# Performance work log

Measured on AMD Instinct MI355X. Metric: run time of the kernel, lower is better.

## Reference

```python
import jax, jax.numpy as jnp
import numpy as np

N = 50000      # nodes
E = 800000     # edges
IN = 64        # in_channels
HID = 128      # hidden_channels
HEADS = 4
D = HID // HEADS  # 32 per-head dim
G = 64         # graphs in batch


def setup_inputs() -> dict:
    key = jax.random.key(0)
    ks = jax.random.split(key, 24)
    def p(k, shape):
        return (jax.random.normal(k, shape, jnp.float32) * 0.05)
    x = jax.random.normal(ks[0], (N, IN), jnp.float32)
    edge_index = jax.random.randint(ks[1], (2, E), 0, N, dtype=jnp.int32).astype(jnp.int64)
    batch = jnp.sort(jax.random.randint(ks[2], (N,), 0, G, dtype=jnp.int32)).astype(jnp.int64)
    inp = {"x": x, "edge_index": edge_index, "batch": batch}
    # layer 1: in -> HID (heads*D), with root/skip projection
    inp["Wq1"] = p(ks[3], (IN, HID)); inp["bq1"] = p(ks[4], (HID,))
    inp["Wk1"] = p(ks[5], (IN, HID)); inp["bk1"] = p(ks[6], (HID,))
    inp["Wv1"] = p(ks[7], (IN, HID)); inp["bv1"] = p(ks[8], (HID,))
    inp["Ws1"] = p(ks[9], (IN, HID)); inp["bs1"] = p(ks[10], (HID,))
    # layer 2: HID -> HID
    inp["Wq2"] = p(ks[11], (HID, HID)); inp["bq2"] = p(ks[12], (HID,))
    inp["Wk2"] = p(ks[13], (HID, HID)); inp["bk2"] = p(ks[14], (HID,))
    inp["Wv2"] = p(ks[15], (HID, HID)); inp["bv2"] = p(ks[16], (HID,))
    inp["Ws2"] = p(ks[17], (HID, HID)); inp["bs2"] = p(ks[18], (HID,))
    # readout linear HID -> 2
    inp["Wl"] = p(ks[19], (HID, 2)); inp["bl"] = p(ks[20], (2,))
    return inp


def transformer_conv(x, src, dst, Wq, bq, Wk, bk, Wv, bv, Ws, bs):
    """PyG TransformerConv (concat=True, root_weight=True, beta=False, eval mode)."""
    n = x.shape[0]
    q = (x @ Wq + bq).reshape(n, HEADS, D)
    k = (x @ Wk + bk).reshape(n, HEADS, D)
    v = (x @ Wv + bv).reshape(n, HEADS, D)
    # per-edge attention logits: query at target (dst), key/value at source (src)
    qi, kj, vj = q[dst], k[src], v[src]           # [E, H, D]
    logits = jnp.sum(qi * kj, axis=-1) / jnp.sqrt(jnp.asarray(D, x.dtype))  # [E, H]
    # segment softmax over incoming edges of each target node
    m = jax.ops.segment_max(logits, dst, num_segments=n)   # [N, H]
    p = jnp.exp(logits - m[dst])                           # [E, H]
    s = jax.ops.segment_sum(p, dst, num_segments=n)        # [N, H]
    alpha = p / s[dst]                                     # [E, H]
    agg = jax.ops.segment_sum(alpha[..., None] * vj, dst, num_segments=n)  # [N, H, D]
    out = agg.reshape(n, HID) + (x @ Ws + bs)              # concat heads + skip
    return out


def reference(x, edge_index, batch,
              Wq1, bq1, Wk1, bk1, Wv1, bv1, Ws1, bs1,
              Wq2, bq2, Wk2, bk2, Wv2, bv2, Ws2, bs2,
              Wl, bl):
    src, dst = edge_index[0], edge_index[1]
    h = jax.nn.relu(transformer_conv(x, src, dst, Wq1, bq1, Wk1, bk1, Wv1, bv1, Ws1, bs1))
    h = jax.nn.relu(transformer_conv(h, src, dst, Wq2, bq2, Wk2, bk2, Wv2, bv2, Ws2, bs2))
    # global mean pool per graph
    counts = jax.ops.segment_sum(jnp.ones((h.shape[0],), h.dtype), batch, num_segments=G)
    pooled = jax.ops.segment_sum(h, batch, num_segments=G) / jnp.maximum(counts, 1.0)[:, None]
    return pooled @ Wl + bl  # [G, 2]
```

## Files before the change

### kernel.cpp

```cpp
#include <hip/hip_runtime.h>
#include <hip/hip_bf16.h>
#include <cstdint>
#include <cstddef>

#define N_NODES 50000
#define N_EDGES 800000
#define IN_CH 64
#define HID_CH 128
#define N_GRAPHS 64

#define NB_SCAN ((N_NODES + 255) / 256)
#define NB_CNT4 ((N_EDGES + 1023) / 1024)
#define NB_GEMM ((N_NODES + 63) / 64)
#define W_ELEMS (4 * IN_CH * 128 + 4 * HID_CH * 128)
#define NB_CONV ((W_ELEMS + 255) / 256)

typedef short s16x8 __attribute__((ext_vector_type(8)));
typedef float f32x4 __attribute__((ext_vector_type(4)));
typedef float f32x2 __attribute__((ext_vector_type(2)));

__device__ __forceinline__ float bf2f(__hip_bfloat16 v) { return __bfloat162float(v); }
__device__ __forceinline__ float bfbits2f(unsigned hs) {
  union { unsigned u; float f; } v; v.u = hs << 16; return v.f;
}
__device__ __forceinline__ float bfhi2f(unsigned w) {
  union { unsigned u; float f; } v; v.u = w & 0xffff0000u; return v.f;
}
__device__ __forceinline__ short f2bfs(float f) {
  __hip_bfloat16 h = __float2bfloat16(f); return *(short*)&h;
}
__device__ __forceinline__ unsigned short f2bfu(float f) {
  __hip_bfloat16 h = __float2bfloat16(f); return *(unsigned short*)&h;
}
__device__ __forceinline__ int clamp_id(int v) {
  if (v < 0) v = 0;
  if (v >= N_NODES) v = N_NODES - 1;
  return v;
}

__device__ __forceinline__ unsigned char f2fp8(float v) {
  return (unsigned char)(__builtin_amdgcn_cvt_pk_fp8_f32(v, v, 0, false) & 0xff);
}
template<bool HI>
__device__ __forceinline__ f32x2 fp8pair(unsigned w) {
  return __builtin_amdgcn_cvt_pk_f32_fp8(w, HI);
}

__device__ __forceinline__ f32x2 pkfma(f32x2 a, f32x2 b, f32x2 c) {
  f32x2 d;
  asm("v_pk_fma_f32 %0, %1, %2, %3" : "=v"(d) : "v"(a), "v"(b), "v"(c));
  return d;
}
__device__ __forceinline__ f32x2 pkadd(f32x2 a, f32x2 b) {
  f32x2 d;
  asm("v_pk_add_f32 %0, %1, %2" : "=v"(d) : "v"(a), "v"(b));
  return d;
}

__global__ __launch_bounds__(256)
void prep(const int* __restrict__ ei, int* __restrict__ cnt,
          unsigned short* __restrict__ rank,
          const float* __restrict__ w1q, const float* __restrict__ w1k,
          const float* __restrict__ w1v, const float* __restrict__ w1s,
          const float* __restrict__ w2q, const float* __restrict__ w2k,
          const float* __restrict__ w2v, const float* __restrict__ w2s,
          __hip_bfloat16* d1q, __hip_bfloat16* d1k, __hip_bfloat16* d1v, __hip_bfloat16* d1s,
          __hip_bfloat16* d2q, __hip_bfloat16* d2k, __hip_bfloat16* d2v, __hip_bfloat16* d2s)
{
  int bx = blockIdx.x;
  if (bx < NB_CNT4) {
    int e0 = bx * 1024 + threadIdx.x * 4;
    if (e0 >= N_EDGES) return;
    if (e0 + 3 < N_EDGES) {
      int4 dv = *(const int4*)(ei + N_EDGES + e0);
      unsigned short r0 = (unsigned short)atomicAdd(&cnt[clamp_id(dv.x)], 1);
      unsigned short r1 = (unsigned short)atomicAdd(&cnt[clamp_id(dv.y)], 1);
      unsigned short r2 = (unsigned short)atomicAdd(&cnt[clamp_id(dv.z)], 1);
      unsigned short r3 = (unsigned short)atomicAdd(&cnt[clamp_id(dv.w)], 1);
      ushort4 rv; rv.x = r0; rv.y = r1; rv.z = r2; rv.w = r3;
      *(ushort4*)(rank + e0) = rv;
    } else {
      for (int j = 0; j < 4; ++j)
        if (e0 + j < N_EDGES)
          rank[e0 + j] = (unsigned short)atomicAdd(&cnt[clamp_id(ei[N_EDGES + e0 + j])], 1);
    }
    return;
  }
  int j = (bx - NB_CNT4) * 256 + threadIdx.x;
  if (j >= W_ELEMS) return;
  const float* S[8] = {w1q, w1k, w1v, w1s, w2q, w2k, w2v, w2s};
  __hip_bfloat16* D[8] = {d1q, d1k, d1v, d1s, d2q, d2k, d2v, d2s};
  int m, r;
  if (j < 4 * IN_CH * 128) { m = j >> 13; r = j & 8191; }
  else { int jj = j - 4 * IN_CH * 128; m = 4 + (jj >> 14); r = jj & 16383; }
  int k = r >> 7, c = r & 127;
  D[m][(((k >> 3) * 128 + c) << 3) + (k & 7)] = __float2bfloat16(S[m][r]);
}

template<int KD, int XF32>
__device__ __forceinline__ void gemm_body(
    int bg, const void* X,
    const short* __restrict__ WTq, const short* __restrict__ WTk,
    const short* __restrict__ WTv, const short* __restrict__ WTs,
    const float* __restrict__ bq, const float* __restrict__ bk,
    const float* __restrict__ bv, const float* __restrict__ bs,
    short* Qo, unsigned char* KV8, short* So, short* lds)
{
  constexpr int KT = KD / 32;
  constexpr int CHUNKS = KD * 16;
  const int tid  = threadIdx.x;
  const int wid  = tid >> 6;
  const int lane = tid & 63;
  const int quad = lane >> 4;
  const int mm   = lane & 15;
  const int rt   = wid & 1;
  const int ch   = wid >> 1;
  const int rowbase = bg * 64 + rt * 32;

  s16x8 afrag[2][KT];
  #pragma unroll
  for (int t = 0; t < 2; ++t) {
    const int arow = rowbase + t * 16 + mm;
    if (arow < N_NODES) {
      if (XF32) {
        const float* xp = (const float*)X + (size_t)arow * KD;
        #pragma unroll
        for (int kt = 0; kt < KT; ++kt) {
          const float4* p = (const float4*)(xp + kt * 32 + quad * 8);
          float4 a = p[0], b = p[1];
          s16x8 fr;
          fr[0] = f2bfs(a.x); fr[1] = f2bfs(a.y); fr[2] = f2bfs(a.z); fr[3] = f2bfs(a.w);
          fr[4] = f2bfs(b.x); fr[5] = f2bfs(b.y); fr[6] = f2bfs(b.z); fr[7] = f2bfs(b.w);
          afrag[t][kt] = fr;
        }
      } else {
        const short* xp = (const short*)X + (size_t)arow * KD;
        #pragma unroll
        for (int kt = 0; kt < KT; ++kt)
          afrag[t][kt] = *(const s16x8*)(xp + kt * 32 + quad * 8);
      }
    } else {
      #pragma unroll
      for (int kt = 0; kt < KT; ++kt)
        afrag[t][kt] = (s16x8){0,0,0,0,0,0,0,0};
    }
  }

  const short* wts[4] = {WTq, WTk, WTv, WTs};
  const float* bias[4] = {bq, bk, bv, bs};

  #pragma unroll
  for (int mat = 0; mat < 4; ++mat) {
    if (mat > 0) __syncthreads();
    {
      const uint4* src = (const uint4*)wts[mat];
      uint4* dst = (uint4*)lds;
      #pragma unroll
      for (int i = 0; i < CHUNKS / 256; ++i)
        dst[tid + i * 256] = src[tid + i * 256];
    }
    __syncthreads();

    f32x4 acc[4][2];
    #pragma unroll
    for (int c4 = 0; c4 < 4; ++c4) {
      float b = bias[mat][ch * 64 + c4 * 16 + mm];
      f32x4 av = {b, b, b, b};
      acc[c4][0] = av; acc[c4][1] = av;
    }
    #pragma unroll
    for (int kt = 0; kt < KT; ++kt) {
      #pragma unroll
      for (int c4 = 0; c4 < 4; ++c4) {
        s16x8 bfrag = *(const s16x8*)(lds + ((((kt * 4 + quad) << 7) + ch * 64 + c4 * 16 + mm) << 3));
        acc[c4][0] = __builtin_amdgcn_mfma_f32_16x16x32_bf16(afrag[0][kt], bfrag, acc[c4][0], 0, 0, 0);
        acc[c4][1] = __builtin_amdgcn_mfma_f32_16x16x32_bf16(afrag[1][kt], bfrag, acc[c4][1], 0, 0, 0);
      }
    }
    if (mat == 1 || mat == 2) {
      unsigned char* O8 = KV8 + ((mat == 1) ? 0 : 128);
      #pragma unroll
      for (int c4 = 0; c4 < 4; ++c4) {
        const int col = ch * 64 + c4 * 16 + mm;
        #pragma unroll
        for (int t = 0; t < 2; ++t) {
          #pragma unroll
          for (int r = 0; r < 4; ++r) {
            int row = rowbase + t * 16 + quad * 4 + r;
            if (row < N_NODES)
              O8[(size_t)row * 256 + col] = f2fp8(acc[c4][t][r]);
          }
        }
      }
    } else {
      short* O = (mat == 0) ? Qo : So;
      #pragma unroll
      for (int c4 = 0; c4 < 4; ++c4) {
        const int col = ch * 64 + c4 * 16 + mm;
        #pragma unroll
        for (int t = 0; t < 2; ++t) {
          #pragma unroll
          for (int r = 0; r < 4; ++r) {
            int row = rowbase + t * 16 + quad * 4 + r;
            if (row < N_NODES)
              ((__hip_bfloat16*)O)[(size_t)row * 128 + col] = __float2bfloat16(acc[c4][t][r]);
          }
        }
      }
    }
  }
}

__global__ __launch_bounds__(256)
void scan1(const int* __restrict__ cnt, int* __restrict__ offs, int* __restrict__ bsum) {
  __shared__ int wsum[4];
  int t = threadIdx.x, lane = t & 63, w = t >> 6;
  int i = blockIdx.x * 256 + t;
  int v = (i < N_NODES) ? cnt[i] : 0;
  int x = v;
  #pragma unroll
  for (int o = 1; o < 64; o <<= 1) { int y = __shfl_up(x, o, 64); if (lane >= o) x += y; }
  if (lane == 63) wsum[w] = x;
  __syncthreads();
  if (t == 0) {
    int run = 0;
    #pragma unroll
    for (int k = 0; k < 4; ++k) { int tv = wsum[k]; wsum[k] = run; run += tv; }
    bsum[blockIdx.x] = run;
  }
  __syncthreads();
  if (i <= N_NODES) offs[i] = wsum[w] + x - v;
}

__global__ __launch_bounds__(256)
void scan2(int* __restrict__ bsum) {
  __shared__ int wsum[4];
  int t = threadIdx.x, lane = t & 63, w = t >> 6;
  int v = (t < NB_SCAN) ? bsum[t] : 0;
  int x = v;
  #pragma unroll
  for (int o = 1; o < 64; o <<= 1) { int y = __shfl_up(x, o, 64); if (lane >= o) x += y; }
  if (lane == 63) wsum[w] = x;
  __syncthreads();
  if (t == 0) {
    int run = 0;
    #pragma unroll
    for (int k = 0; k < 4; ++k) { int tv = wsum[k]; wsum[k] = run; run += tv; }
  }
  __syncthreads();
  if (t < NB_SCAN) bsum[t] = wsum[w] + x - v;
}

__global__ __launch_bounds__(256)
void scatter_gemm1(const int* __restrict__ ei, const int* __restrict__ offs,
                   const int* __restrict__ bsum, const unsigned short* __restrict__ rank,
                   int* __restrict__ ssrc,
                   const float* __restrict__ X,
                   const short* __restrict__ w1q, const short* __restrict__ w1k,
                   const short* __restrict__ w1v, const short* __restrict__ w1s,
                   const float* __restrict__ b1q, const float* __restrict__ b1k,
                   const float* __restrict__ b1v, const float* __restrict__ b1s,
                   short* Qb, unsigned char* KV8, short* Sb)
{
  __shared__ short lds[IN_CH * 128];
  int bx = blockIdx.x;
  if (bx >= NB_GEMM) {
    int e0 = (bx - NB_GEMM) * 1024 + threadIdx.x * 4;
    if (e0 >= N_EDGES) return;
    if (e0 + 3 < N_EDGES) {
      int4 sv = *(const int4*)(ei + e0);
      int4 dv = *(const int4*)(ei + N_EDGES + e0);
      ushort4 rv = *(const ushort4*)(rank + e0);
      int d0 = clamp_id(dv.x), d1 = clamp_id(dv.y);
      int d2 = clamp_id(dv.z), d3 = clamp_id(dv.w);
      int p0 = offs[d0] + bsum[d0 >> 8] + rv.x;
      int p1 = offs[d1] + bsum[d1 >> 8] + rv.y;
      int p2 = offs[d2] + bsum[d2 >> 8] + rv.z;
      int p3 = offs[d3] + bsum[d3 >> 8] + rv.w;
      ssrc[p0] = clamp_id(sv.x);
      ssrc[p1] = clamp_id(sv.y);
      ssrc[p2] = clamp_id(sv.z);
      ssrc[p3] = clamp_id(sv.w);
    } else {
      for (int j = 0; j < 4; ++j) {
        int e = e0 + j;
        if (e < N_EDGES) {
          int src = clamp_id(ei[e]);
          int dst = clamp_id(ei[N_EDGES + e]);
          ssrc[offs[dst] + bsum[dst >> 8] + rank[e]] = src;
        }
      }
    }
    return;
  }
  gemm_body<IN_CH, 1>(bx, X, w1q, w1k, w1v, w1s, b1q, b1k, b1v, b1s,
                      Qb, KV8, Sb, lds);
}

__global__ __launch_bounds__(256)
void attn_kernel(const unsigned short* __restrict__ Q, const unsigned char* __restrict__ KV8,
                 const unsigned short* S,
                 const int* __restrict__ offs, const int* __restrict__ bsum,
                 const int* __restrict__ ssrc, unsigned short* H)
{
  const int dst = blockIdx.x * 4 + (threadIdx.x >> 6);
  if (dst >= N_NODES) return;
  const int lane = threadIdx.x & 63;
  const int sub  = lane >> 4;
  const int cl   = lane & 15;

  const float qs = 0.17677669529663687f * 1.4426950408889634f;
  uint4 qw = *(const uint4*)(Q + (size_t)dst * 128 + cl * 8);
  f32x2 q2[4], a2[4];
  #pragma unroll
  for (int i = 0; i < 4; ++i) {
    unsigned w = ((unsigned*)&qw)[i];
    f32x2 t; t.x = bfbits2f(w & 0xffffu) * qs; t.y = bfhi2f(w) * qs;
    q2[i] = t;
    a2[i].x = 0.f; a2[i].y = 0.f;
  }
  float s = 0.f;

  const int e0 = offs[dst] + bsum[dst >> 8];
  const int e1 = offs[dst + 1] + bsum[(dst + 1) >> 8];
  const int iters = (e1 - e0 + 3) >> 2;

  if (iters > 0) {
    int e = e0 + sub;
    bool have = (e < e1);
    int src = have ? ssrc[e] : ssrc[e0];
    float ph = have ? 1.f : 0.f;
    const unsigned char* kvp = KV8 + (size_t)src * 256 + cl * 8;
    uint2 kw = *(const uint2*)(kvp);
    uint2 vw = *(const uint2*)(kvp + 128);

    for (int it = 0; it < iters; ++it) {
      uint2 kwn, vwn;
      int en = e + 4;
      bool haven = (en < e1);
      float phn = haven ? 1.f : 0.f;
      if (it + 1 < iters) {
        int srcn = haven ? ssrc[en] : ssrc[e0];
        const unsigned char* kvn = KV8 + (size_t)srcn * 256 + cl * 8;
        kwn = *(const uint2*)(kvn);
        vwn = *(const uint2*)(kvn + 128);
      } else {
        kwn = kw; vwn = vw;
      }
      f32x2 k0 = fp8pair<false>(kw.x), k1 = fp8pair<true>(kw.x);
      f32x2 k2 = fp8pair<false>(kw.y), k3 = fp8pair<true>(kw.y);
      f32x2 zz; zz.x = 0.f; zz.y = 0.f;
      f32x2 dd = pkfma(q2[0], k0, zz);
      dd = pkfma(q2[1], k1, dd);
      dd = pkfma(q2[2], k2, dd);
      dd = pkfma(q2[3], k3, dd);
      float d = dd.x + dd.y;
      d += __shfl_xor(d, 1, 64);
      d += __shfl_xor(d, 2, 64);
      float p = exp2f(d) * ph;
      s += p;
      f32x2 p2; p2.x = p; p2.y = p;
      f32x2 v0 = fp8pair<false>(vw.x), v1 = fp8pair<true>(vw.x);
      f32x2 v2 = fp8pair<false>(vw.y), v3 = fp8pair<true>(vw.y);
      a2[0] = pkfma(p2, v0, a2[0]);
      a2[1] = pkfma(p2, v1, a2[1]);
      a2[2] = pkfma(p2, v2, a2[2]);
      a2[3] = pkfma(p2, v3, a2[3]);
      kw = kwn; vw = vwn; ph = phn; e = en;
    }
  }

  s += __shfl_xor(s, 16, 64);
  s += __shfl_xor(s, 32, 64);
  #pragma unroll
  for (int i = 0; i < 4; ++i) {
    f32x2 t;
    t.x = __shfl_xor(a2[i].x, 16, 64);
    t.y = __shfl_xor(a2[i].y, 16, 64);
    a2[i] = pkadd(a2[i], t);
    t.x = __shfl_xor(a2[i].x, 32, 64);
    t.y = __shfl_xor(a2[i].y, 32, 64);
    a2[i] = pkadd(a2[i], t);
  }
  const float inv = (s > 0.f) ? (1.0f / s) : 0.f;

  if (sub == 0) {
    uint4 sw = *(const uint4*)(S + (size_t)dst * 128 + cl * 8);
    uint4 ow;
    #pragma unroll
    for (int i = 0; i < 4; ++i) {
      unsigned w = ((unsigned*)&sw)[i];
      float o0 = fmaxf(a2[i].x * inv + bfbits2f(w & 0xffffu), 0.f);
      float o1 = fmaxf(a2[i].y * inv + bfhi2f(w), 0.f);
      ((unsigned*)&ow)[i] = (unsigned)f2bfu(o0) | ((unsigned)f2bfu(o1) << 16);
    }
    *(uint4*)(H + (size_t)dst * 128 + cl * 8) = ow;
  }
}

__global__ __launch_bounds__(256)
void gemm2(const short* __restrict__ X,
           const short* __restrict__ w2q, const short* __restrict__ w2k,
           const short* __restrict__ w2v, const short* __restrict__ w2s,
           const float* __restrict__ b2q, const float* __restrict__ b2k,
           const float* __restrict__ b2v, const float* __restrict__ b2s,
           short* Qb, unsigned char* KV8, short* Sb)
{
  __shared__ short lds[HID_CH * 128];
  gemm_body<HID_CH, 0>(blockIdx.x, X, w2q, w2k, w2v, w2s, b2q, b2k, b2v, b2s,
                       Qb, KV8, Sb, lds);
}

__device__ __forceinline__ int lower_bound_i(const int* __restrict__ b, int n, int val) {
  int lo = 0, hi = n;
  while (lo < hi) { int mid = (lo + hi) >> 1; if (b[mid] < val) lo = mid + 1; else hi = mid; }
  return lo;
}

__global__ __launch_bounds__(128)
void pool_partial(const __hip_bfloat16* __restrict__ H, const int* __restrict__ batch,
                  float* __restrict__ pooled)
{
  const int g = blockIdx.x >> 4, p = blockIdx.x & 15, t = threadIdx.x;
  const int s = lower_bound_i(batch, N_NODES, g);
  const int e = lower_bound_i(batch, N_NODES, g + 1);
  const int len = e - s;
  if (len <= 0) return;
  const int chunk = (len + 15) >> 4;
  const int a = s + p * chunk;
  const int b = min(a + chunk, e);
  if (a >= b) return;
  float sum = 0.f;
  for (int i = a; i < b; ++i) sum += bf2f(H[(size_t)i * 128 + t]);
  atomicAdd(&pooled[g * 128 + t], sum);
}

__global__ __launch_bounds__(128)
void pool_final(const float* __restrict__ pooled, const int* __restrict__ batch,
                const float* __restrict__ Wl, const float* __restrict__ bl,
                float* __restrict__ out)
{
  const int g = blockIdx.x, t = threadIdx.x;
  __shared__ float r0[128], r1[128];
  const int s = lower_bound_i(batch, N_NODES, g);
  const int e = lower_bound_i(batch, N_NODES, g + 1);
  const float inv = 1.0f / (float)max(e - s, 1);
  const float pc = pooled[g * 128 + t] * inv;
  r0[t] = pc * Wl[t * 2 + 0];
  r1[t] = pc * Wl[t * 2 + 1];
  __syncthreads();
  for (int o = 64; o > 0; o >>= 1) {
    if (t < o) { r0[t] += r0[t + o]; r1[t] += r1[t + o]; }
    __syncthreads();
  }
  if (t == 0) {
    out[g * 2 + 0] = r0[0] + bl[0];
    out[g * 2 + 1] = r1[0] + bl[1];
  }
}


extern "C" void kernel_launch(void* const* d_in, const int* in_sizes, int n_in,
                              void* d_out, int out_size, void* d_ws, size_t ws_size,
                              hipStream_t stream) {
  uintptr_t base = (uintptr_t)d_ws;
  auto take = [&](size_t bytes) -> uintptr_t {
    uintptr_t p = base;
    base += (bytes + 255) & ~(size_t)255;
    return p;
  };

  int*   cnt    = (int*)take((size_t)N_NODES * 4);
  float* pooled = (float*)take((size_t)N_GRAPHS * 128 * 4);
  int*   offs   = (int*)take((size_t)(N_NODES + 1) * 4);
  int*   bsum   = (int*)take((size_t)NB_SCAN * 4);
  int*   ssrc   = (int*)take((size_t)N_EDGES * 4);
  unsigned short* rank = (unsigned short*)take((size_t)N_EDGES * 2);
  short* Qb     = (short*)take((size_t)N_NODES * 128 * 2);
  unsigned char* KV8 = (unsigned char*)take((size_t)N_NODES * 256);
  short* Sb     = (short*)take((size_t)N_NODES * 128 * 2);
  short* wt1q   = (short*)take((size_t)IN_CH * 128 * 2);
  short* wt1k   = (short*)take((size_t)IN_CH * 128 * 2);
  short* wt1v   = (short*)take((size_t)IN_CH * 128 * 2);
  short* wt1s   = (short*)take((size_t)IN_CH * 128 * 2);
  short* wt2q   = (short*)take((size_t)HID_CH * 128 * 2);
  short* wt2k   = (short*)take((size_t)HID_CH * 128 * 2);
  short* wt2v   = (short*)take((size_t)HID_CH * 128 * 2);
  short* wt2s   = (short*)take((size_t)HID_CH * 128 * 2);

  const int* ei    = (const int*)d_in[1];
  const int* batch = (const int*)d_in[2];

  size_t zspan = (size_t)((char*)pooled + (size_t)N_GRAPHS * 128 * 4 - (char*)cnt);
  hipMemsetAsync(cnt, 0, zspan, stream);

  prep<<<NB_CNT4 + NB_CONV, 256, 0, stream>>>(
      ei, cnt, rank,
      (const float*)d_in[3], (const float*)d_in[5], (const float*)d_in[7], (const float*)d_in[9],
      (const float*)d_in[11], (const float*)d_in[13], (const float*)d_in[15], (const float*)d_in[17],
      (__hip_bfloat16*)wt1q, (__hip_bfloat16*)wt1k, (__hip_bfloat16*)wt1v, (__hip_bfloat16*)wt1s,
      (__hip_bfloat16*)wt2q, (__hip_bfloat16*)wt2k, (__hip_bfloat16*)wt2v, (__hip_bfloat16*)wt2s);

  scan1<<<NB_SCAN, 256, 0, stream>>>(cnt, offs, bsum);
  scan2<<<1, 256, 0, stream>>>(bsum);

  scatter_gemm1<<<NB_GEMM + NB_CNT4, 256, 0, stream>>>(
      ei, offs, bsum, rank, ssrc,
      (const float*)d_in[0],
      wt1q, wt1k, wt1v, wt1s,
      (const float*)d_in[4], (const float*)d_in[6], (const float*)d_in[8], (const float*)d_in[10],
      Qb, KV8, Sb);

  const int attn_grid = (N_NODES + 3) / 4;

  attn_kernel<<<attn_grid, 256, 0, stream>>>(
      (const unsigned short*)Qb, KV8,
      (const unsigned short*)Sb, offs, bsum, ssrc, (unsigned short*)Sb);

  gemm2<<<NB_GEMM, 256, 0, stream>>>(
      Sb, wt2q, wt2k, wt2v, wt2s,
      (const float*)d_in[12], (const float*)d_in[14], (const float*)d_in[16], (const float*)d_in[18],
      Qb, KV8, Sb);

  attn_kernel<<<attn_grid, 256, 0, stream>>>(
      (const unsigned short*)Qb, KV8,
      (const unsigned short*)Sb, offs, bsum, ssrc, (unsigned short*)Sb);

  pool_partial<<<N_GRAPHS * 16, 128, 0, stream>>>(
      (const __hip_bfloat16*)Sb, batch, pooled);
  pool_final<<<N_GRAPHS, 128, 0, stream>>>(pooled, batch, (const float*)d_in[19],
                                           (const float*)d_in[20], (float*)d_out);
}
```

Measured before the change: 293.2 us.

## Interleave fp8 K/V per lane chunk and use DPP quad reduction

The projection epilogue now stores K and V interleaved in 16-byte chunks (8 K bytes followed by 8 V bytes per 8 columns), so the edge aggregation loop fetches both with one 128-bit gather instead of two 64-bit gathers. The 4-lane dot-product reduction uses DPP moves in place of shuffles. This is meant to cut gather instruction count and cross-lane latency in the edge loop, at the cost of a more scattered byte-store pattern in the GEMM epilogue.

Result: no change. 292.3 us (-0.3%).

```diff
diff --git a/kernel.cpp b/kernel.cpp
--- a/kernel.cpp
+++ b/kernel.cpp
@@ -54,6 +54,12 @@
 __device__ __forceinline__ f32x2 pkadd(f32x2 a, f32x2 b) {
   f32x2 d;
   asm("v_pk_add_f32 %0, %1, %2" : "=v"(d) : "v"(a), "v"(b));
+  return d;
+}
+
+__device__ __forceinline__ float quad_sum(float d) {
+  d += __int_as_float(__builtin_amdgcn_mov_dpp(__float_as_int(d), 0xB1, 0xf, 0xf, true));
+  d += __int_as_float(__builtin_amdgcn_mov_dpp(__float_as_int(d), 0x4E, 0xf, 0xf, true));
   return d;
 }
 
@@ -178,17 +184,18 @@
       }
     }
     if (mat == 1 || mat == 2) {
-      unsigned char* O8 = KV8 + ((mat == 1) ? 0 : 128);
+      const int voff = (mat == 2) ? 8 : 0;
       #pragma unroll
       for (int c4 = 0; c4 < 4; ++c4) {
         const int col = ch * 64 + c4 * 16 + mm;
+        const int bpos = ((col >> 3) << 4) + voff + (col & 7);
         #pragma unroll
         for (int t = 0; t < 2; ++t) {
           #pragma unroll
           for (int r = 0; r < 4; ++r) {
             int row = rowbase + t * 16 + quad * 4 + r;
             if (row < N_NODES)
-              O8[(size_t)row * 256 + col] = f2fp8(acc[c4][t][r]);
+              KV8[(size_t)row * 256 + bpos] = f2fp8(acc[c4][t][r]);
           }
         }
       }
@@ -330,43 +337,37 @@
     bool have = (e < e1);
     int src = have ? ssrc[e] : ssrc[e0];
     float ph = have ? 1.f : 0.f;
-    const unsigned char* kvp = KV8 + (size_t)src * 256 + cl * 8;
-    uint2 kw = *(const uint2*)(kvp);
-    uint2 vw = *(const uint2*)(kvp + 128);
+    uint4 kv = *(const uint4*)(KV8 + (size_t)src * 256 + cl * 16);
 
     for (int it = 0; it < iters; ++it) {
-      uint2 kwn, vwn;
+      uint4 kvn;
       int en = e + 4;
       bool haven = (en < e1);
       float phn = haven ? 1.f : 0.f;
       if (it + 1 < iters) {
         int srcn = haven ? ssrc[en] : ssrc[e0];
-        const unsigned char* kvn = KV8 + (size_t)srcn * 256 + cl * 8;
-        kwn = *(const uint2*)(kvn);
-        vwn = *(const uint2*)(kvn + 128);
+        kvn = *(const uint4*)(KV8 + (size_t)srcn * 256 + cl * 16);
       } else {
-        kwn = kw; vwn = vw;
+        kvn = kv;
       }
-      f32x2 k0 = fp8pair<false>(kw.x), k1 = fp8pair<true>(kw.x);
-      f32x2 k2 = fp8pair<false>(kw.y), k3 = fp8pair<true>(kw.y);
+      f32x2 k0 = fp8pair<false>(kv.x), k1 = fp8pair<true>(kv.x);
+      f32x2 k2 = fp8pair<false>(kv.y), k3 = fp8pair<true>(kv.y);
       f32x2 zz; zz.x = 0.f; zz.y = 0.f;
       f32x2 dd = pkfma(q2[0], k0, zz);
       dd = pkfma(q2[1], k1, dd);
       dd = pkfma(q2[2], k2, dd);
       dd = pkfma(q2[3], k3, dd);
-      float d = dd.x + dd.y;
-      d += __shfl_xor(d, 1, 64);
-      d += __shfl_xor(d, 2, 64);
+      float d = quad_sum(dd.x + dd.y);
       float p = exp2f(d) * ph;
       s += p;
       f32x2 p2; p2.x = p; p2.y = p;
-      f32x2 v0 = fp8pair<false>(vw.x), v1 = fp8pair<true>(vw.x);
-      f32x2 v2 = fp8pair<false>(vw.y), v3 = fp8pair<true>(vw.y);
+      f32x2 v0 = fp8pair<false>(kv.z), v1 = fp8pair<true>(kv.z);
+      f32x2 v2 = fp8pair<false>(kv.w), v3 = fp8pair<true>(kv.w);
       a2[0] = pkfma(p2, v0, a2[0]);
       a2[1] = pkfma(p2, v1, a2[1]);
       a2[2] = pkfma(p2, v2, a2[2]);
       a2[3] = pkfma(p2, v3, a2[3]);
-      kw = kwn; vw = vwn; ph = phn; e = en;
+      kv = kvn; ph = phn; e = en;
     }
   }
 
```
